# Kernel tuning notes

Hardware: AMD Instinct MI355X
Metric: run time of the kernel (lower is better)

The kernel has to match this reference:

```python
import jax, jax.numpy as jnp
from jax import lax
import numpy as np

B, T, C = 8, 16384, 64
NUM_FILTERS, FILTER_SIZE = 64, 5
LEAKY_SLOPE = 0.3  # keras activation 'leaky_relu' default negative_slope


def setup_inputs() -> dict:
    key = jax.random.key(0)
    k1, k2, k3 = jax.random.split(key, 3)
    x = jax.random.normal(k1, (B, T, C), dtype=jnp.float32)
    interp_weights = jax.random.normal(k2, (C,), dtype=jnp.float32)
    # Conv1D kernel layout: [filter_size, in_channels, out_channels]
    conv_kernel = jax.random.normal(k3, (FILTER_SIZE, C, NUM_FILTERS), dtype=jnp.float32) * 0.05
    conv_bias = jnp.zeros((NUM_FILTERS,), dtype=jnp.float32)
    return {"x": x, "interp_weights": interp_weights,
            "conv_kernel": conv_kernel, "conv_bias": conv_bias}


def reference(x, interp_weights, conv_kernel, conv_bias):
    # Sigmoid gate per channel
    w = jax.nn.sigmoid(interp_weights)  # [C]
    # The diag conv2d (filter [1,2,C,C], SAME) is: blend[t] = w*x[t] + (1-w)*x[t+1]
    # (TF SAME for even width pads one zero frame on the right)
    x_next = jnp.concatenate([x[:, 1:, :], jnp.zeros_like(x[:, :1, :])], axis=1)
    blend = w * x + (1.0 - w) * x_next  # [B, T, C]
    # Interleave: even positions original, odd positions blended -> [B, 2T, C]
    up = jnp.stack([x, blend], axis=2).reshape(B, 2 * T, C)
    # Conv1D(num_filters, filter_size, padding='same', stride 1) + leaky_relu
    y = lax.conv_general_dilated(
        up, conv_kernel,
        window_strides=(1,), padding='SAME',
        dimension_numbers=('NWC', 'WIO', 'NWC'))
    y = y + conv_bias
    return jnp.where(y >= 0, y, LEAKY_SLOPE * y)
```

## Files before the change

### kernel.cpp

```cpp
#include <hip/hip_runtime.h>
#include <hip/hip_bf16.h>
#include <cstdint>


#define T_ 16384
#define TWO_T 32768
#define RING 40

typedef __bf16 bf16x8 __attribute__((ext_vector_type(8)));
typedef float  f32x4  __attribute__((ext_vector_type(4)));
typedef unsigned short u16x8 __attribute__((ext_vector_type(8)));

__device__ __forceinline__ float sigmoidf_(float z) {
    return 1.0f / (1.0f + expf(-z));
}

__device__ __forceinline__ unsigned short f2bf(float f) {
    union { float f; uint32_t u; } v; v.f = f;
    uint32_t u = v.u;
    return (unsigned short)((u + 0x7FFFu + ((u >> 16) & 1u)) >> 16);
}

__global__ void lu_prep_kernel(const float* __restrict__ iw,
                               const float* __restrict__ ck,
                               const float* __restrict__ x,
                               unsigned short* __restrict__ bp,
                               float* __restrict__ corrf,
                               float* __restrict__ zp) {
    int fi = blockIdx.x;
    int l  = threadIdx.x;
    if (fi < 56) {
        int phase, ks, nt;
        if (fi < 24) { phase = 0; ks = fi >> 2; nt = fi & 3; }
        else         { phase = 1; ks = (fi - 24) >> 2; nt = (fi - 24) & 3; }
        int tap = ks >> 1;
        int n   = nt * 16 + (l & 15);
        int c0  = ((ks & 1) << 5) + ((l >> 4) << 3);
        u16x8 pk;
#pragma unroll
        for (int i = 0; i < 8; ++i) {
            int c = c0 + i;
            float w = sigmoidf_(iw[c]);
            float v;
            #define CK(k) ck[((k) * 64 + c) * 64 + n]
            if (phase == 0) {
                if (tap == 0)      v = CK(0) + w * CK(1);
                else if (tap == 1) v = (1.f - w) * CK(1) + CK(2) + w * CK(3);
                else               v = (1.f - w) * CK(3) + CK(4);
            } else {
                if (tap == 0)      v = w * CK(0);
                else if (tap == 1) v = (1.f - w) * CK(0) + CK(1) + w * CK(2);
                else if (tap == 2) v = (1.f - w) * CK(2) + CK(3) + w * CK(4);
                else               v = (1.f - w) * CK(4);
            }
            #undef CK
            pk[i] = f2bf(v);
        }
        *(u16x8*)(bp + (((size_t)fi * 64) + l) * 8) = pk;
    } else {
        int b = fi - 56;
        int f = l;
        float cE = 0.f, cO = 0.f;
#pragma unroll
        for (int c = 0; c < 64; ++c) {
            float w = sigmoidf_(iw[c]);
            float g = (1.f - w) * x[(size_t)b * T_ * 64 + c];
            cE += ck[(64 + c) * 64 + f] * g;
            cO += ck[c * 64 + f] * g;
        }
        corrf[b * 128 + f]      = cE;
        corrf[b * 128 + 64 + f] = cO;
        if (fi == 63) zp[l] = 0.f;
    }
}

__device__ __forceinline__ void gload16(const float* g, float* l) {
    __builtin_amdgcn_global_load_lds(
        (const __attribute__((address_space(1))) uint32_t*)g,
        (__attribute__((address_space(3))) uint32_t*)l, 16, 0, 0);
}

__device__ __forceinline__ void stage4(const float* __restrict__ xb,
                                       const float* __restrict__ zp,
                                       int p0, int S, int lane, float* xw) {
    int fr = S + (lane >> 4);
    int f  = p0 + fr - 1;
    int ch = (lane & 15) ^ ((fr - 1) & 7);
    const float* gp = ((unsigned)f < (unsigned)T_)
                    ? xb + ((size_t)f << 6) + (ch << 2)
                    : zp + (ch << 2);
    gload16(gp, xw + ((S % RING) << 6));
}

__device__ __forceinline__ bf16x8 pack8(f32x4 a, f32x4 b) {
    bf16x8 r;
    r[0] = (__bf16)a[0]; r[1] = (__bf16)a[1];
    r[2] = (__bf16)a[2]; r[3] = (__bf16)a[3];
    r[4] = (__bf16)b[0]; r[5] = (__bf16)b[1];
    r[6] = (__bf16)b[2]; r[7] = (__bf16)b[3];
    return r;
}

__global__ __launch_bounds__(256, 4) void lu_main_kernel(
        const float* __restrict__ x,
        const unsigned short* __restrict__ bp,
        const float* __restrict__ corrf,
        const float* __restrict__ bias,
        const float* __restrict__ zp,
        float* __restrict__ out) {
    __shared__ __align__(16) float xl[4][RING * 64];

    const int bid  = blockIdx.x;
    const int b    = bid >> 8;
    const int q    = bid & 255;
    const int p0   = q << 6;
    const int lane = threadIdx.x & 63;
    const int wv   = threadIdx.x >> 6;

    float* xw = &xl[wv][0];
    const float* xb = x + (size_t)b * T_ * 64;

    bf16x8 We[6], Wo[8];
#pragma unroll
    for (int ks = 0; ks < 6; ++ks)
        We[ks] = __builtin_bit_cast(bf16x8,
            *(const u16x8*)(bp + (((size_t)(ks * 4 + wv)) * 64 + lane) * 8));
#pragma unroll
    for (int ks = 0; ks < 8; ++ks)
        Wo[ks] = __builtin_bit_cast(bf16x8,
            *(const u16x8*)(bp + (((size_t)(24 + ks * 4 + wv)) * 64 + lane) * 8));

    const int hi   = lane >> 4;
    const int hi2  = hi << 1;
    const int col  = lane & 15;
    const float4 bias4 = *(const float4*)(bias + (wv << 4) + (hi << 2));
    const char* xwb = (const char*)xw;

#pragma unroll
    for (int k = 0; k < 5; ++k) stage4(xb, zp, p0, k * 4, lane, xw);

#pragma unroll
    for (int w = 0; w < 4; ++w) {
        if (w < 3) {
#pragma unroll
            for (int k = 0; k < 4; ++k)
                stage4(xb, zp, p0, 20 + (w << 4) + (k << 2), lane, xw);
        }

        if (w == 0)      asm volatile("s_waitcnt vmcnt(4)" ::: "memory");
        else if (w < 3)  asm volatile("s_waitcnt vmcnt(6)" ::: "memory");
        else             asm volatile("s_waitcnt vmcnt(2)" ::: "memory");
        __builtin_amdgcn_sched_barrier(0);

        f32x4 accE = {0.f, 0.f, 0.f, 0.f};
        f32x4 accO = {0.f, 0.f, 0.f, 0.f};
#pragma unroll
        for (int tap = 0; tap < 4; ++tap) {
            int fr  = (w << 4) + col + tap;
            int row = fr - (fr >= RING ? RING : 0);
            int key = (fr - 1) & 7;
            int off0 = (row << 8) + ((hi2 ^ key) << 4);
            f32x4 qa = *(const f32x4*)(xwb + off0);
            f32x4 qb = *(const f32x4*)(xwb + (off0 ^ 16));
            f32x4 qc = *(const f32x4*)(xwb + off0 + 128);
            f32x4 qd = *(const f32x4*)(xwb + ((off0 + 128) ^ 16));
            bf16x8 x0 = pack8(qa, qb);
            bf16x8 x1 = pack8(qc, qd);
            if (tap < 3) {
                accE = __builtin_amdgcn_mfma_f32_16x16x32_bf16(We[tap * 2],     x0, accE, 0, 0, 0);
                accE = __builtin_amdgcn_mfma_f32_16x16x32_bf16(We[tap * 2 + 1], x1, accE, 0, 0, 0);
            }
            accO = __builtin_amdgcn_mfma_f32_16x16x32_bf16(Wo[tap * 2],     x0, accO, 0, 0, 0);
            accO = __builtin_amdgcn_mfma_f32_16x16x32_bf16(Wo[tap * 2 + 1], x1, accO, 0, 0, 0);
        }

        if (((q | w) == 0) && col == 0) {
            const float4 cE4 = *(const float4*)(corrf + b * 128 + (wv << 4) + (hi << 2));
            const float4 cO4 = *(const float4*)(corrf + b * 128 + 64 + (wv << 4) + (hi << 2));
            accE[0] -= cE4.x; accE[1] -= cE4.y; accE[2] -= cE4.z; accE[3] -= cE4.w;
            accO[0] -= cO4.x; accO[1] -= cO4.y; accO[2] -= cO4.z; accO[3] -= cO4.w;
        }

        const int tl = p0 + (w << 4) + col;
        const size_t fbase = ((size_t)b * TWO_T + ((size_t)tl << 1)) * 64
                           + (wv << 4) + (hi << 2);
        float4 vE, vO;
        {
            float e0 = accE[0] + bias4.x, e1 = accE[1] + bias4.y,
                  e2 = accE[2] + bias4.z, e3 = accE[3] + bias4.w;
            vE.x = e0 >= 0.f ? e0 : 0.3f * e0;
            vE.y = e1 >= 0.f ? e1 : 0.3f * e1;
            vE.z = e2 >= 0.f ? e2 : 0.3f * e2;
            vE.w = e3 >= 0.f ? e3 : 0.3f * e3;
            float o0 = accO[0] + bias4.x, o1 = accO[1] + bias4.y,
                  o2 = accO[2] + bias4.z, o3 = accO[3] + bias4.w;
            vO.x = o0 >= 0.f ? o0 : 0.3f * o0;
            vO.y = o1 >= 0.f ? o1 : 0.3f * o1;
            vO.z = o2 >= 0.f ? o2 : 0.3f * o2;
            vO.w = o3 >= 0.f ? o3 : 0.3f * o3;
        }
        *(float4*)(out + fbase)      = vE;
        *(float4*)(out + fbase + 64) = vO;
    }
}

extern "C" void kernel_launch(void* const* d_in, const int* in_sizes, int n_in,
                              void* d_out, int out_size, void* d_ws, size_t ws_size,
                              hipStream_t stream) {
    (void)in_sizes; (void)n_in; (void)out_size; (void)ws_size;
    const float* x    = (const float*)d_in[0];
    const float* iw   = (const float*)d_in[1];
    const float* ck   = (const float*)d_in[2];
    const float* bias = (const float*)d_in[3];
    float* out = (float*)d_out;
    unsigned short* bp = (unsigned short*)d_ws;
    float* corrf = (float*)((char*)d_ws + 57344);
    float* zp    = (float*)((char*)d_ws + 61440);

    lu_prep_kernel<<<64, 64, 0, stream>>>(iw, ck, x, bp, corrf, zp);
    lu_main_kernel<<<2048, 256, 0, stream>>>(x, bp, corrf, bias, zp, out);
}
```

Baseline: 33.22 us.

## Share one block-wide x tile in LDS instead of per-wave ring buffers

Before, each of the four waves staged all 67 input frames into its own 40-row ring buffer, overlapping loads with MFMA through manual vmcnt waits. Now the block loads the 68-frame window once into a shared LDS tile, with each wave loading a quarter, then does a __syncthreads before computing. This cuts global and LDS traffic to a quarter and uses less LDS, which could allow more resident blocks. The cost is losing per-wave load/compute overlap and adding a block-wide barrier.

Result: faster. 32.02 us (-3.6%).

```diff
diff --git a/kernel.cpp b/kernel.cpp
--- a/kernel.cpp
+++ b/kernel.cpp
@@ -5,7 +5,7 @@
 
 #define T_ 16384
 #define TWO_T 32768
-#define RING 40
+#define NFR 68
 
 typedef __bf16 bf16x8 __attribute__((ext_vector_type(8)));
 typedef float  f32x4  __attribute__((ext_vector_type(4)));
@@ -80,18 +80,6 @@
         (__attribute__((address_space(3))) uint32_t*)l, 16, 0, 0);
 }
 
-__device__ __forceinline__ void stage4(const float* __restrict__ xb,
-                                       const float* __restrict__ zp,
-                                       int p0, int S, int lane, float* xw) {
-    int fr = S + (lane >> 4);
-    int f  = p0 + fr - 1;
-    int ch = (lane & 15) ^ ((fr - 1) & 7);
-    const float* gp = ((unsigned)f < (unsigned)T_)
-                    ? xb + ((size_t)f << 6) + (ch << 2)
-                    : zp + (ch << 2);
-    gload16(gp, xw + ((S % RING) << 6));
-}
-
 __device__ __forceinline__ bf16x8 pack8(f32x4 a, f32x4 b) {
     bf16x8 r;
     r[0] = (__bf16)a[0]; r[1] = (__bf16)a[1];
@@ -108,7 +96,7 @@
         const float* __restrict__ bias,
         const float* __restrict__ zp,
         float* __restrict__ out) {
-    __shared__ __align__(16) float xl[4][RING * 64];
+    __shared__ __align__(16) float xl[NFR * 64];
 
     const int bid  = blockIdx.x;
     const int b    = bid >> 8;
@@ -117,7 +105,6 @@
     const int lane = threadIdx.x & 63;
     const int wv   = threadIdx.x >> 6;
 
-    float* xw = &xl[wv][0];
     const float* xb = x + (size_t)b * T_ * 64;
 
     bf16x8 We[6], Wo[8];
@@ -134,32 +121,34 @@
     const int hi2  = hi << 1;
     const int col  = lane & 15;
     const float4 bias4 = *(const float4*)(bias + (wv << 4) + (hi << 2));
-    const char* xwb = (const char*)xw;
-
-#pragma unroll
-    for (int k = 0; k < 5; ++k) stage4(xb, zp, p0, k * 4, lane, xw);
+
+#pragma unroll
+    for (int g = 0; g < 5; ++g) {
+        int j0 = g * 16 + (wv << 2);
+        if (j0 < NFR) {
+            int j  = j0 + (lane >> 4);
+            int gf = p0 - 1 + j;
+            int ch = (lane & 15) ^ (j & 7);
+            const float* gp = ((unsigned)gf < (unsigned)T_)
+                            ? xb + ((size_t)gf << 6) + (ch << 2)
+                            : zp + (ch << 2);
+            gload16(gp, xl + j0 * 64);
+        }
+    }
+
+    __syncthreads();
+
+    const char* xwb = (const char*)xl;
 
 #pragma unroll
     for (int w = 0; w < 4; ++w) {
-        if (w < 3) {
-#pragma unroll
-            for (int k = 0; k < 4; ++k)
-                stage4(xb, zp, p0, 20 + (w << 4) + (k << 2), lane, xw);
-        }
-
-        if (w == 0)      asm volatile("s_waitcnt vmcnt(4)" ::: "memory");
-        else if (w < 3)  asm volatile("s_waitcnt vmcnt(6)" ::: "memory");
-        else             asm volatile("s_waitcnt vmcnt(2)" ::: "memory");
-        __builtin_amdgcn_sched_barrier(0);
-
         f32x4 accE = {0.f, 0.f, 0.f, 0.f};
         f32x4 accO = {0.f, 0.f, 0.f, 0.f};
 #pragma unroll
         for (int tap = 0; tap < 4; ++tap) {
-            int fr  = (w << 4) + col + tap;
-            int row = fr - (fr >= RING ? RING : 0);
-            int key = (fr - 1) & 7;
-            int off0 = (row << 8) + ((hi2 ^ key) << 4);
+            int j    = (w << 4) + col + tap;
+            int key  = j & 7;
+            int off0 = (j << 8) + ((hi2 ^ key) << 4);
             f32x4 qa = *(const f32x4*)(xwb + off0);
             f32x4 qb = *(const f32x4*)(xwb + (off0 ^ 16));
             f32x4 qc = *(const f32x4*)(xwb + off0 + 128);
```
